# Kernel tuning notes

Measured on AMD Instinct MI355X. Metric: run time of the kernel, lower is better.

The kernel has to match this reference:

```python
import jax, jax.numpy as jnp
import numpy as np

B, N, D, H = 1, 4096, 512, 8
HD = D // H


def setup_inputs() -> dict:
    key = jax.random.key(0)
    ks = jax.random.split(key, 12)
    s = 0.02  # weight init scale for numerical stability
    query = jax.random.normal(ks[0], (B, N, D), jnp.float32)
    key_t = jax.random.normal(ks[1], (B, N, D), jnp.float32)
    value = jax.random.normal(ks[2], (B, N, D), jnp.float32)
    Wq = jax.random.normal(ks[3], (D, D), jnp.float32) * s
    bq = jax.random.normal(ks[4], (D,), jnp.float32) * s
    Wk = jax.random.normal(ks[5], (D, D), jnp.float32) * s
    bk = jax.random.normal(ks[6], (D,), jnp.float32) * s
    Wv = jax.random.normal(ks[7], (D, D), jnp.float32) * s
    bv = jax.random.normal(ks[8], (D,), jnp.float32) * s
    Wo = jax.random.normal(ks[9], (D, D), jnp.float32) * s
    bo = jax.random.normal(ks[10], (D,), jnp.float32) * s
    # build sgconv_mat exactly as __init__: shifted nonneg adjacency, max-normalized,
    # then symmetric degree normalization D^-1/2 A D^-1/2 (gwmha_layer_num=1)
    A = jax.random.uniform(ks[11], (N, N), jnp.float32)
    A = A + A.min()
    A = A / A.max()
    deg = A.sum(1)
    dinv = 1.0 / jnp.sqrt(deg)
    sgconv_mat = (dinv[:, None] * A * dinv[None, :])[None]  # [1,N,N]
    return {"query": query, "key": key_t, "value": value,
            "Wq": Wq, "bq": bq, "Wk": Wk, "bk": bk, "Wv": Wv, "bv": bv,
            "Wo": Wo, "bo": bo, "sgconv_mat": sgconv_mat}


def reference(query, key, value, Wq, bq, Wk, bk, Wv, bv, Wo, bo, sgconv_mat):
    b, n, d = query.shape
    q = (query @ Wq.T + bq).reshape(b, n, H, HD)
    k = (key @ Wk.T + bk).reshape(b, n, H, HD)
    v = (value @ Wv.T + bv).reshape(b, n, H, HD)
    energy = jnp.einsum('bqhd,bkhd->bhqk', q, k)
    attn = jax.nn.softmax(energy / jnp.sqrt(jnp.float32(d)), axis=3)
    out = jnp.einsum('bhqk,bkhd->bqhd', attn, v).reshape(b, n, d)
    out = sgconv_mat @ out          # [1,N,N] @ [B,N,D] -> [B,N,D]
    return out @ Wo.T + bo
```

## Files before the change

### kernel.cpp

```cpp
#include <hip/hip_runtime.h>
#include <hip/hip_bf16.h>
#include <math.h>

typedef __bf16 bf16_t;
typedef __bf16 bf16x8 __attribute__((ext_vector_type(8)));
typedef unsigned short ushort8v __attribute__((ext_vector_type(8)));
typedef float floatx4 __attribute__((ext_vector_type(4)));

static __device__ inline unsigned short f2bf_rne(float f) {
    unsigned int u = __builtin_bit_cast(unsigned int, f);
    unsigned int r = u + 0x7FFFu + ((u >> 16) & 1u);
    return (unsigned short)(r >> 16);
}
static __device__ inline bf16_t f2bf(float f) {
    return __builtin_bit_cast(bf16_t, f2bf_rne(f));
}

static __device__ inline void store_c(float* C, size_t i, float v) { C[i] = v; }
static __device__ inline void store_c(bf16_t* C, size_t i, float v) { C[i] = f2bf(v); }

static __device__ inline void cvt8(const float* src, bf16_t* dst, size_t idx) {
    float4 a = *(const float4*)(src + idx);
    float4 c = *(const float4*)(src + idx + 4);
    ushort8v u;
    u[0] = f2bf_rne(a.x); u[1] = f2bf_rne(a.y); u[2] = f2bf_rne(a.z); u[3] = f2bf_rne(a.w);
    u[4] = f2bf_rne(c.x); u[5] = f2bf_rne(c.y); u[6] = f2bf_rne(c.z); u[7] = f2bf_rne(c.w);
    *(ushort8v*)(dst + idx) = u;
}

template <typename TC>
__device__ inline void gemm_body(
    const bf16_t* __restrict__ A, int lda,
    const bf16_t* __restrict__ B, int ldb,
    const float* __restrict__ bias_col, const float* __restrict__ bias_row,
    TC* __restrict__ C, int ldc, int K, int m0, int n0)
{
    __shared__ bf16_t As[128 * 68];
    __shared__ bf16_t Bs[64 * 68];

    const int tid = threadIdx.x;
    const int lane = tid & 63, wave = tid >> 6;
    const int wm = wave & 1, wn = wave >> 1;
    const int lo16 = lane & 15, quad = lane >> 4;
    const int sr = tid >> 2, sc = (tid & 3) * 8;

    floatx4 acc[4][2] = {};

    for (int k0 = 0; k0 < K; k0 += 32) {
        bf16x8 a0 = *(const bf16x8*)(A + (size_t)(m0 + sr) * lda + k0 + sc);
        bf16x8 a1 = *(const bf16x8*)(A + (size_t)(m0 + 64 + sr) * lda + k0 + sc);
        bf16x8 b0 = *(const bf16x8*)(B + (size_t)(n0 + sr) * ldb + k0 + sc);
        __syncthreads();
        *(bf16x8*)(&As[sr * 68 + sc]) = a0;
        *(bf16x8*)(&As[(64 + sr) * 68 + sc]) = a1;
        *(bf16x8*)(&Bs[sr * 68 + sc]) = b0;
        __syncthreads();

        bf16x8 af[4], bfv[2];
#pragma unroll
        for (int mt = 0; mt < 4; ++mt)
            af[mt] = *(const bf16x8*)(&As[(wm * 64 + mt * 16 + lo16) * 68 + quad * 8]);
#pragma unroll
        for (int nt = 0; nt < 2; ++nt)
            bfv[nt] = *(const bf16x8*)(&Bs[(wn * 32 + nt * 16 + lo16) * 68 + quad * 8]);
#pragma unroll
        for (int mt = 0; mt < 4; ++mt)
#pragma unroll
            for (int nt = 0; nt < 2; ++nt)
                acc[mt][nt] = __builtin_amdgcn_mfma_f32_16x16x32_bf16(
                    af[mt], bfv[nt], acc[mt][nt], 0, 0, 0);
    }

#pragma unroll
    for (int nt = 0; nt < 2; ++nt) {
        const int gn = n0 + wn * 32 + nt * 16 + lo16;
        const float bc = bias_col ? bias_col[gn] : 0.f;
#pragma unroll
        for (int mt = 0; mt < 4; ++mt) {
#pragma unroll
            for (int r = 0; r < 4; ++r) {
                const int gm = m0 + wm * 64 + mt * 16 + quad * 4 + r;
                float v = acc[mt][nt][r] + bc;
                if (bias_row) v += bias_row[gm];
                store_c(C, (size_t)gm * ldc + gn, v);
            }
        }
    }
}

__global__ __launch_bounds__(256) void prep(
    const float* __restrict__ query, const float* __restrict__ key, const float* __restrict__ value,
    const float* __restrict__ Wq, const float* __restrict__ Wk,
    const float* __restrict__ Wv, const float* __restrict__ Wo,
    bf16_t* qB, bf16_t* kB, bf16_t* vB,
    bf16_t* wqB, bf16_t* wkB, bf16_t* wvB, bf16_t* woB)
{
    const int b = blockIdx.x;
    const float* src; bf16_t* dst; size_t base;
    if      (b < 256) { src = query; dst = qB;  base = (size_t)b * 8192; }
    else if (b < 512) { src = key;   dst = kB;  base = (size_t)(b - 256) * 8192; }
    else if (b < 768) { src = value; dst = vB;  base = (size_t)(b - 512) * 8192; }
    else if (b < 800) { src = Wq;    dst = wqB; base = (size_t)(b - 768) * 8192; }
    else if (b < 832) { src = Wk;    dst = wkB; base = (size_t)(b - 800) * 8192; }
    else if (b < 864) { src = Wv;    dst = wvB; base = (size_t)(b - 832) * 8192; }
    else              { src = Wo;    dst = woB; base = (size_t)(b - 864) * 8192; }
#pragma unroll
    for (int it = 0; it < 4; ++it)
        cvt8(src, dst, base + (size_t)it * 2048 + threadIdx.x * 8);
}

__global__ __launch_bounds__(256) void proj_qkv(
    const bf16_t* __restrict__ qB, const bf16_t* __restrict__ wqB, const float* __restrict__ bq,
    const bf16_t* __restrict__ kB, const bf16_t* __restrict__ wkB, const float* __restrict__ bk,
    const bf16_t* __restrict__ wvB, const bf16_t* __restrict__ vB, const float* __restrict__ bv,
    bf16_t* __restrict__ q, bf16_t* __restrict__ k, bf16_t* __restrict__ vt)
{
    const int b = blockIdx.x;
    const bf16_t *A, *B;
    const float *bc = nullptr, *br = nullptr;
    bf16_t* C;
    int ldc = 512, m0, n0;
    if (b < 512) {
        int i = b & 255, x = i & 7, t = i >> 3;
        n0 = (t & 7) * 64;
        m0 = ((t >> 3) * 8 + x) * 128;
        if (b < 256) { A = qB; B = wqB; bc = bq; C = q; }
        else         { A = kB; B = wkB; bc = bk; C = k; }
    } else {
        int i = b - 512;
        n0 = (i & 63) * 64;
        m0 = (i >> 6) * 128;
        A = wvB; B = vB; br = bv; C = vt; ldc = 4096;
    }
    gemm_body<bf16_t>(A, 512, B, 512, bc, br, C, ldc, 512, m0, n0);
}

__global__ __launch_bounds__(256) void sgconv_gemm(
    const bf16_t* __restrict__ sgb, const bf16_t* __restrict__ aot,
    float* __restrict__ part)
{
    const int i = blockIdx.x & 255;
    const int kb = blockIdx.x >> 8;
    const int ms = i & 31, ns = i >> 5;
    const int m0 = ms * 128, n0 = ns * 64;
    const int kbase = kb * 1024;
    gemm_body<float>(sgb + kbase, 4096, aot + kbase, 4096, nullptr, nullptr,
                     part + (size_t)kb * (4096 * 512), 512, 1024, m0, n0);
}

__global__ __launch_bounds__(256) void part_reduce(
    const float* __restrict__ p, bf16_t* __restrict__ o2)
{
    const size_t S = (size_t)4096 * 512;
    const size_t idx = ((size_t)blockIdx.x * 256 + threadIdx.x) * 8;
    ushort8v u;
#pragma unroll
    for (int half = 0; half < 2; ++half) {
        float4 s = *(const float4*)(p + idx + half * 4);
#pragma unroll
        for (int kb = 1; kb < 4; ++kb) {
            float4 t = *(const float4*)(p + kb * S + idx + half * 4);
            s.x += t.x; s.y += t.y; s.z += t.z; s.w += t.w;
        }
        u[half * 4 + 0] = f2bf_rne(s.x);
        u[half * 4 + 1] = f2bf_rne(s.y);
        u[half * 4 + 2] = f2bf_rne(s.z);
        u[half * 4 + 3] = f2bf_rne(s.w);
    }
    *(ushort8v*)(o2 + idx) = u;
}

__global__ __launch_bounds__(256) void out_proj(
    const bf16_t* __restrict__ o2, const bf16_t* __restrict__ woB,
    const float* __restrict__ bo, float* __restrict__ out)
{
    const int i = blockIdx.x, x = i & 7, t = i >> 3;
    const int n0 = (t & 7) * 64;
    const int m0 = ((t >> 3) * 8 + x) * 64;

    __shared__ bf16_t As[64 * 68];
    __shared__ bf16_t Bs[64 * 68];

    const int tid = threadIdx.x;
    const int lane = tid & 63, wave = tid >> 6;
    const int wm = wave & 1, wn = wave >> 1;
    const int lo16 = lane & 15, quad = lane >> 4;
    const int sr = tid >> 2, sc = (tid & 3) * 8;

    floatx4 acc[2][2] = {};

    for (int k0 = 0; k0 < 512; k0 += 32) {
        bf16x8 a0 = *(const bf16x8*)(o2 + (size_t)(m0 + sr) * 512 + k0 + sc);
        bf16x8 b0 = *(const bf16x8*)(woB + (size_t)(n0 + sr) * 512 + k0 + sc);
        __syncthreads();
        *(bf16x8*)(&As[sr * 68 + sc]) = a0;
        *(bf16x8*)(&Bs[sr * 68 + sc]) = b0;
        __syncthreads();

        bf16x8 af[2], bfv[2];
#pragma unroll
        for (int mt = 0; mt < 2; ++mt)
            af[mt] = *(const bf16x8*)(&As[(wm * 32 + mt * 16 + lo16) * 68 + quad * 8]);
#pragma unroll
        for (int nt = 0; nt < 2; ++nt)
            bfv[nt] = *(const bf16x8*)(&Bs[(wn * 32 + nt * 16 + lo16) * 68 + quad * 8]);
#pragma unroll
        for (int mt = 0; mt < 2; ++mt)
#pragma unroll
            for (int nt = 0; nt < 2; ++nt)
                acc[mt][nt] = __builtin_amdgcn_mfma_f32_16x16x32_bf16(
                    af[mt], bfv[nt], acc[mt][nt], 0, 0, 0);
    }

#pragma unroll
    for (int nt = 0; nt < 2; ++nt) {
        const int gn = n0 + wn * 32 + nt * 16 + lo16;
        const float bc = bo[gn];
#pragma unroll
        for (int mt = 0; mt < 2; ++mt)
#pragma unroll
            for (int r = 0; r < 4; ++r) {
                const int gm = m0 + wm * 32 + mt * 16 + quad * 4 + r;
                out[(size_t)gm * 512 + gn] = acc[mt][nt][r] + bc;
            }
    }
}

__global__ __launch_bounds__(256, 4) void flash_attn(
    const bf16_t* __restrict__ q, const bf16_t* __restrict__ kk,
    const bf16_t* __restrict__ vt, float* __restrict__ op,
    float* __restrict__ lp, float scale,
    const float* __restrict__ sg, bf16_t* __restrict__ sgb)
{
    if (blockIdx.x >= 1024) {
        const size_t base = (size_t)(blockIdx.x - 1024) * 8192;
#pragma unroll
        for (int it = 0; it < 4; ++it)
            cvt8(sg, sgb, base + (size_t)it * 2048 + threadIdx.x * 8);
        return;
    }

    const int N = 4096, D = 512;
    const int h   = blockIdx.x & 7;
    const int qb  = (blockIdx.x >> 3) & 31;
    const int qtr = blockIdx.x >> 8;
    const int t0  = qtr * 1024;

    const int tid = threadIdx.x;
    const int w = tid >> 6, lane = tid & 63;
    const int lo16 = lane & 15, quad = lane >> 4;

    __shared__ bf16_t Ks[64 * 72];
    __shared__ bf16_t Vs[64 * 72];
    __shared__ bf16_t Ps[4][32 * 72];

    const bf16_t* qp = q + (size_t)(qb * 128 + w * 32 + lo16) * D + h * 64 + quad * 8;
    bf16x8 qf[2][2];
    qf[0][0] = *(const bf16x8*)qp;
    qf[0][1] = *(const bf16x8*)(qp + 32);
    qf[1][0] = *(const bf16x8*)(qp + 16 * D);
    qf[1][1] = *(const bf16x8*)(qp + 16 * D + 32);

    const int srow = tid >> 2, sc = (tid & 3) * 16;
    const bf16_t* ksrc = kk + (size_t)(t0 + srow) * D + h * 64 + sc;
    const bf16_t* vsrc = vt + (size_t)(h * 64 + srow) * N + t0 + sc;
    bf16_t* kdst = &Ks[srow * 72 + sc];
    bf16_t* vdst = &Vs[srow * 72 + sc];

    floatx4 o[4][2] = {};
    float l[2] = {0.f, 0.f};

    bf16x8 kr0 = *(const bf16x8*)ksrc;
    bf16x8 kr1 = *(const bf16x8*)(ksrc + 8);
    bf16x8 vr0 = *(const bf16x8*)vsrc;
    bf16x8 vr1 = *(const bf16x8*)(vsrc + 8);

    for (int it = 0; it < 16; ++it) {
        __syncthreads();
        *(bf16x8*)kdst = kr0;  *(bf16x8*)(kdst + 8) = kr1;
        *(bf16x8*)vdst = vr0;  *(bf16x8*)(vdst + 8) = vr1;
        __syncthreads();
        if (it < 15) {
            const bf16_t* kn = ksrc + (size_t)(it + 1) * 64 * D;
            const bf16_t* vn = vsrc + (it + 1) * 64;
            kr0 = *(const bf16x8*)kn;  kr1 = *(const bf16x8*)(kn + 8);
            vr0 = *(const bf16x8*)vn;  vr1 = *(const bf16x8*)(vn + 8);
        }

        floatx4 s[4][2];
#pragma unroll
        for (int tt = 0; tt < 4; ++tt) {
            bf16x8 kf0 = *(const bf16x8*)(&Ks[(tt * 16 + lo16) * 72 + quad * 8]);
            bf16x8 kf1 = *(const bf16x8*)(&Ks[(tt * 16 + lo16) * 72 + 32 + quad * 8]);
#pragma unroll
            for (int qt = 0; qt < 2; ++qt) {
                floatx4 a = {};
                a = __builtin_amdgcn_mfma_f32_16x16x32_bf16(kf0, qf[qt][0], a, 0, 0, 0);
                a = __builtin_amdgcn_mfma_f32_16x16x32_bf16(kf1, qf[qt][1], a, 0, 0, 0);
                s[tt][qt] = a;
            }
        }
#pragma unroll
        for (int tt = 0; tt < 4; ++tt)
#pragma unroll
            for (int qt = 0; qt < 2; ++qt) {
                float e0 = __expf(s[tt][qt][0] * scale);
                float e1 = __expf(s[tt][qt][1] * scale);
                float e2 = __expf(s[tt][qt][2] * scale);
                float e3 = __expf(s[tt][qt][3] * scale);
                l[qt] += (e0 + e1) + (e2 + e3);
                uint2 pk;
                pk.x = (unsigned)f2bf_rne(e0) | ((unsigned)f2bf_rne(e1) << 16);
                pk.y = (unsigned)f2bf_rne(e2) | ((unsigned)f2bf_rne(e3) << 16);
                *(uint2*)(&Ps[w][(qt * 16 + lo16) * 72 + tt * 16 + quad * 4]) = pk;
            }
#pragma unroll
        for (int ks = 0; ks < 2; ++ks) {
            bf16x8 pf0 = *(const bf16x8*)(&Ps[w][lo16 * 72 + ks * 32 + quad * 8]);
            bf16x8 pf1 = *(const bf16x8*)(&Ps[w][(16 + lo16) * 72 + ks * 32 + quad * 8]);
#pragma unroll
            for (int t = 0; t < 4; ++t) {
                bf16x8 vf = *(const bf16x8*)(&Vs[(t * 16 + lo16) * 72 + ks * 32 + quad * 8]);
                o[t][0] = __builtin_amdgcn_mfma_f32_16x16x32_bf16(vf, pf0, o[t][0], 0, 0, 0);
                o[t][1] = __builtin_amdgcn_mfma_f32_16x16x32_bf16(vf, pf1, o[t][1], 0, 0, 0);
            }
        }
    }

#pragma unroll
    for (int qt = 0; qt < 2; ++qt) {
        l[qt] += __shfl_xor(l[qt], 16);
        l[qt] += __shfl_xor(l[qt], 32);
    }

    const int g = blockIdx.x & 255;
    float* opw = op + ((size_t)qtr * 256 + g) * 8192;
#pragma unroll
    for (int t = 0; t < 4; ++t)
#pragma unroll
        for (int pt = 0; pt < 2; ++pt)
#pragma unroll
            for (int r = 0; r < 4; ++r)
                opw[(t * 16 + quad * 4 + r) * 128 + w * 32 + pt * 16 + lo16] = o[t][pt][r];

    if (quad == 0) {
        float* lpw = lp + ((size_t)qtr * 256 + g) * 128;
        lpw[w * 32 + lo16] = l[0];
        lpw[w * 32 + 16 + lo16] = l[1];
    }
}

__global__ __launch_bounds__(256) void attn_combine(
    const float* __restrict__ op, const float* __restrict__ lp, bf16_t* __restrict__ aot)
{
    const int g = blockIdx.x;
    const int h = g & 7, qb = g >> 3;
    const int tid = threadIdx.x;
    __shared__ float ls[128];
    if (tid < 128) {
        float s = 0.f;
#pragma unroll
        for (int qtr = 0; qtr < 4; ++qtr)
            s += lp[((size_t)qtr * 256 + g) * 128 + tid];
        ls[tid] = 1.0f / s;
    }
    __syncthreads();
    const float* b0 = op + (size_t)g * 8192;
    const size_t QS = (size_t)256 * 8192;
#pragma unroll 4
    for (int i = 0; i < 32; ++i) {
        int idx = i * 256 + tid;
        float v = b0[idx] + b0[QS + idx] + b0[2 * QS + idx] + b0[3 * QS + idx];
        int dim = idx >> 7, qc = idx & 127;
        aot[(size_t)(h * 64 + dim) * 4096 + qb * 128 + qc] = f2bf(v * ls[qc]);
    }
}

extern "C" void kernel_launch(void* const* d_in, const int* in_sizes, int n_in,
                              void* d_out, int out_size, void* d_ws, size_t ws_size,
                              hipStream_t stream)
{
    const int N = 4096, D = 512;
    const float* query = (const float*)d_in[0];
    const float* key_t = (const float*)d_in[1];
    const float* value = (const float*)d_in[2];
    const float* Wq = (const float*)d_in[3];
    const float* bq = (const float*)d_in[4];
    const float* Wk = (const float*)d_in[5];
    const float* bk = (const float*)d_in[6];
    const float* Wv = (const float*)d_in[7];
    const float* bv = (const float*)d_in[8];
    const float* Wo = (const float*)d_in[9];
    const float* bo = (const float*)d_in[10];
    const float* sg = (const float*)d_in[11];
    float* out = (float*)d_out;

    const size_t ND = (size_t)N * D;
    const size_t DD = (size_t)D * D;

    char* base = (char*)d_ws;
    bf16_t* q    = (bf16_t*)base;
    bf16_t* kk   = q   + ND;
    bf16_t* vt   = kk  + ND;
    bf16_t* aot  = vt  + ND;
    bf16_t* sgb  = aot + ND;
    char* regA   = (char*)(sgb + (size_t)N * N);
    bf16_t* qB   = (bf16_t*)regA;
    bf16_t* kB   = qB + ND;
    bf16_t* vB   = kB + ND;
    bf16_t* wqB  = vB + ND;
    bf16_t* wkB  = wqB + DD;
    bf16_t* wvB  = wkB + DD;
    float* op    = (float*)regA;
    float* p     = (float*)regA;
    char* tail   = regA + (size_t)4 * 256 * 8192 * 4;
    float*  lp   = (float*)tail;
    bf16_t* woB  = (bf16_t*)(lp + (size_t)4 * 256 * 128);
    bf16_t* o2   = woB + DD;

    const dim3 blk(256);

    prep<<<896, blk, 0, stream>>>(query, key_t, value, Wq, Wk, Wv, Wo,
                                  qB, kB, vB, wqB, wkB, wvB, woB);

    proj_qkv<<<768, blk, 0, stream>>>(qB, wqB, bq, kB, wkB, bk,
                                      wvB, vB, bv, q, kk, vt);

    const float scale = 1.0f / sqrtf((float)D);
    flash_attn<<<3072, blk, 0, stream>>>(q, kk, vt, op, lp, scale, sg, sgb);
    attn_combine<<<256, blk, 0, stream>>>(op, lp, aot);

    sgconv_gemm<<<1024, blk, 0, stream>>>(sgb, aot, p);
    part_reduce<<<1024, blk, 0, stream>>>(p, o2);
    out_proj<<<512, blk, 0, stream>>>(o2, woB, bo, out);

    (void)in_sizes; (void)n_in; (void)out_size; (void)ws_size;
}
```

Measured before the change: 252.8 us.

## Use 128x128 GEMM tiles with direct global-to-LDS loads and fold softmax scale

The shared GEMM body now computes 128x128 tiles. It loads operands straight into LDS with global_load_lds, using an XOR-swizzled layout in place of the padded one, and halves the grid sizes for the projection and sgconv GEMMs. The softmax scale and log2(e) are folded into the Q projection, so the attention kernel uses exp2f without a per-element multiply. The hand-written RNE bf16 conversion is swapped for native casts, and the sgconv conversion blocks are interleaved with flash-attention blocks. Larger tiles raise register use and halve the number of workgroups, which could reduce occupancy.

Result: slower. 278.5 us (+10.2%).

```diff
diff --git a/kernel.cpp b/kernel.cpp
--- a/kernel.cpp
+++ b/kernel.cpp
@@ -4,76 +4,101 @@
 
 typedef __bf16 bf16_t;
 typedef __bf16 bf16x8 __attribute__((ext_vector_type(8)));
-typedef unsigned short ushort8v __attribute__((ext_vector_type(8)));
 typedef float floatx4 __attribute__((ext_vector_type(4)));
 
-static __device__ inline unsigned short f2bf_rne(float f) {
-    unsigned int u = __builtin_bit_cast(unsigned int, f);
-    unsigned int r = u + 0x7FFFu + ((u >> 16) & 1u);
-    return (unsigned short)(r >> 16);
-}
-static __device__ inline bf16_t f2bf(float f) {
-    return __builtin_bit_cast(bf16_t, f2bf_rne(f));
+typedef __attribute__((address_space(1))) void gvoid_t;
+typedef __attribute__((address_space(3))) void lvoid_t;
+
+static __device__ __forceinline__ void gload_lds16(const bf16_t* g, const bf16_t* l) {
+    __builtin_amdgcn_global_load_lds((gvoid_t*)(size_t)g,
+                                     (lvoid_t*)(unsigned)(size_t)l,
+                                     16, 0, 0);
+}
+
+static __device__ __forceinline__ unsigned pack_bf2(float lo, float hi) {
+    bf16_t a = (bf16_t)lo, b = (bf16_t)hi;
+    return (unsigned)__builtin_bit_cast(unsigned short, a)
+         | ((unsigned)__builtin_bit_cast(unsigned short, b) << 16);
 }
 
 static __device__ inline void store_c(float* C, size_t i, float v) { C[i] = v; }
-static __device__ inline void store_c(bf16_t* C, size_t i, float v) { C[i] = f2bf(v); }
+static __device__ inline void store_c(bf16_t* C, size_t i, float v) { C[i] = (bf16_t)v; }
 
 static __device__ inline void cvt8(const float* src, bf16_t* dst, size_t idx) {
     float4 a = *(const float4*)(src + idx);
     float4 c = *(const float4*)(src + idx + 4);
-    ushort8v u;
-    u[0] = f2bf_rne(a.x); u[1] = f2bf_rne(a.y); u[2] = f2bf_rne(a.z); u[3] = f2bf_rne(a.w);
-    u[4] = f2bf_rne(c.x); u[5] = f2bf_rne(c.y); u[6] = f2bf_rne(c.z); u[7] = f2bf_rne(c.w);
-    *(ushort8v*)(dst + idx) = u;
+    uint4 u;
+    u.x = pack_bf2(a.x, a.y);
+    u.y = pack_bf2(a.z, a.w);
+    u.z = pack_bf2(c.x, c.y);
+    u.w = pack_bf2(c.z, c.w);
+    *(uint4*)(dst + idx) = u;
 }
 
 template <typename TC>
-__device__ inline void gemm_body(
+__device__ inline void gemm_body128(
     const bf16_t* __restrict__ A, int lda,
     const bf16_t* __restrict__ B, int ldb,
     const float* __restrict__ bias_col, const float* __restrict__ bias_row,
+    float cscale,
     TC* __restrict__ C, int ldc, int K, int m0, int n0)
 {
-    __shared__ bf16_t As[128 * 68];
-    __shared__ bf16_t Bs[64 * 68];
+    __shared__ bf16_t As[128 * 32];
+    __shared__ bf16_t Bs[128 * 32];
 
     const int tid = threadIdx.x;
     const int lane = tid & 63, wave = tid >> 6;
     const int wm = wave & 1, wn = wave >> 1;
     const int lo16 = lane & 15, quad = lane >> 4;
-    const int sr = tid >> 2, sc = (tid & 3) * 8;
-
-    floatx4 acc[4][2] = {};
+
+    const int r0 = tid >> 2;
+    const int s0 = tid & 3;
+    const int c0 = s0 ^ ((r0 >> 1) & 3);
+    const bf16_t* ga0 = A + (size_t)(m0 + r0) * lda + c0 * 8;
+    const bf16_t* ga1 = A + (size_t)(m0 + 64 + r0) * lda + c0 * 8;
+    const bf16_t* gb0 = B + (size_t)(n0 + r0) * ldb + c0 * 8;
+    const bf16_t* gb1 = B + (size_t)(n0 + 64 + r0) * ldb + c0 * 8;
+    const bf16_t* la0 = As + wave * 512;
+    const bf16_t* la1 = As + 2048 + wave * 512;
+    const bf16_t* lb0 = Bs + wave * 512;
+    const bf16_t* lb1 = Bs + 2048 + wave * 512;
+
+    int aoff[4], boff[4];
+#pragma unroll
+    for (int t = 0; t < 4; ++t) {
+        const int ra = wm * 64 + t * 16 + lo16;
+        aoff[t] = ra * 32 + ((quad ^ ((ra >> 1) & 3)) << 3);
+        const int rb = wn * 64 + t * 16 + lo16;
+        boff[t] = rb * 32 + ((quad ^ ((rb >> 1) & 3)) << 3);
+    }
+
+    floatx4 acc[4][4] = {};
 
     for (int k0 = 0; k0 < K; k0 += 32) {
-        bf16x8 a0 = *(const bf16x8*)(A + (size_t)(m0 + sr) * lda + k0 + sc);
-        bf16x8 a1 = *(const bf16x8*)(A + (size_t)(m0 + 64 + sr) * lda + k0 + sc);
-        bf16x8 b0 = *(const bf16x8*)(B + (size_t)(n0 + sr) * ldb + k0 + sc);
-        __syncthreads();
-        *(bf16x8*)(&As[sr * 68 + sc]) = a0;
-        *(bf16x8*)(&As[(64 + sr) * 68 + sc]) = a1;
-        *(bf16x8*)(&Bs[sr * 68 + sc]) = b0;
-        __syncthreads();
-
-        bf16x8 af[4], bfv[2];
+        __syncthreads();
+        gload_lds16(ga0 + k0, la0);
+        gload_lds16(ga1 + k0, la1);
+        gload_lds16(gb0 + k0, lb0);
+        gload_lds16(gb1 + k0, lb1);
+        __syncthreads();
+
+        bf16x8 af[4], bfv[4];
+#pragma unroll
+        for (int t = 0; t < 4; ++t) {
+            af[t]  = *(const bf16x8*)(As + aoff[t]);
+            bfv[t] = *(const bf16x8*)(Bs + boff[t]);
+        }
 #pragma unroll
         for (int mt = 0; mt < 4; ++mt)
-            af[mt] = *(const bf16x8*)(&As[(wm * 64 + mt * 16 + lo16) * 68 + quad * 8]);
-#pragma unroll
-        for (int nt = 0; nt < 2; ++nt)
-            bfv[nt] = *(const bf16x8*)(&Bs[(wn * 32 + nt * 16 + lo16) * 68 + quad * 8]);
-#pragma unroll
-        for (int mt = 0; mt < 4; ++mt)
-#pragma unroll
-            for (int nt = 0; nt < 2; ++nt)
+#pragma unroll
+            for (int nt = 0; nt < 4; ++nt)
                 acc[mt][nt] = __builtin_amdgcn_mfma_f32_16x16x32_bf16(
                     af[mt], bfv[nt], acc[mt][nt], 0, 0, 0);
     }
 
 #pragma unroll
-    for (int nt = 0; nt < 2; ++nt) {
-        const int gn = n0 + wn * 32 + nt * 16 + lo16;
+    for (int nt = 0; nt < 4; ++nt) {
+        const int gn = n0 + wn * 64 + nt * 16 + lo16;
         const float bc = bias_col ? bias_col[gn] : 0.f;
 #pragma unroll
         for (int mt = 0; mt < 4; ++mt) {
@@ -82,7 +107,7 @@
                 const int gm = m0 + wm * 64 + mt * 16 + quad * 4 + r;
                 float v = acc[mt][nt][r] + bc;
                 if (bias_row) v += bias_row[gm];
-                store_c(C, (size_t)gm * ldc + gn, v);
+                store_c(C, (size_t)gm * ldc + gn, v * cscale);
             }
         }
     }
@@ -113,39 +138,32 @@
     const bf16_t* __restrict__ qB, const bf16_t* __restrict__ wqB, const float* __restrict__ bq,
     const bf16_t* __restrict__ kB, const bf16_t* __restrict__ wkB, const float* __restrict__ bk,
     const bf16_t* __restrict__ wvB, const bf16_t* __restrict__ vB, const float* __restrict__ bv,
-    bf16_t* __restrict__ q, bf16_t* __restrict__ k, bf16_t* __restrict__ vt)
+    bf16_t* __restrict__ q, bf16_t* __restrict__ k, bf16_t* __restrict__ vt, float qscale)
 {
     const int b = blockIdx.x;
-    const bf16_t *A, *B;
-    const float *bc = nullptr, *br = nullptr;
-    bf16_t* C;
-    int ldc = 512, m0, n0;
-    if (b < 512) {
-        int i = b & 255, x = i & 7, t = i >> 3;
-        n0 = (t & 7) * 64;
-        m0 = ((t >> 3) * 8 + x) * 128;
-        if (b < 256) { A = qB; B = wqB; bc = bq; C = q; }
-        else         { A = kB; B = wkB; bc = bk; C = k; }
+    const int i = b & 127;
+    if (b < 256) {
+        const int m0 = (i & 31) * 128, n0 = (i >> 5) * 128;
+        if (b < 128)
+            gemm_body128<bf16_t>(qB, 512, wqB, 512, bq, nullptr, qscale, q, 512, 512, m0, n0);
+        else
+            gemm_body128<bf16_t>(kB, 512, wkB, 512, bk, nullptr, 1.f, k, 512, 512, m0, n0);
     } else {
-        int i = b - 512;
-        n0 = (i & 63) * 64;
-        m0 = (i >> 6) * 128;
-        A = wvB; B = vB; br = bv; C = vt; ldc = 4096;
-    }
-    gemm_body<bf16_t>(A, 512, B, 512, bc, br, C, ldc, 512, m0, n0);
+        const int m0 = (i & 3) * 128, n0 = (i >> 2) * 128;
+        gemm_body128<bf16_t>(wvB, 512, vB, 512, nullptr, bv, 1.f, vt, 4096, 512, m0, n0);
+    }
 }
 
 __global__ __launch_bounds__(256) void sgconv_gemm(
     const bf16_t* __restrict__ sgb, const bf16_t* __restrict__ aot,
     float* __restrict__ part)
 {
-    const int i = blockIdx.x & 255;
-    const int kb = blockIdx.x >> 8;
-    const int ms = i & 31, ns = i >> 5;
-    const int m0 = ms * 128, n0 = ns * 64;
+    const int i = blockIdx.x & 127;
+    const int kb = blockIdx.x >> 7;
+    const int m0 = (i & 31) * 128, n0 = (i >> 5) * 128;
     const int kbase = kb * 1024;
-    gemm_body<float>(sgb + kbase, 4096, aot + kbase, 4096, nullptr, nullptr,
-                     part + (size_t)kb * (4096 * 512), 512, 1024, m0, n0);
+    gemm_body128<float>(sgb + kbase, 4096, aot + kbase, 4096, nullptr, nullptr, 1.f,
+                        part + (size_t)kb * (4096 * 512), 512, 1024, m0, n0);
 }
 
 __global__ __launch_bounds__(256) void part_reduce(
@@ -153,7 +171,7 @@
 {
     const size_t S = (size_t)4096 * 512;
     const size_t idx = ((size_t)blockIdx.x * 256 + threadIdx.x) * 8;
-    ushort8v u;
+    uint4 u;
 #pragma unroll
     for (int half = 0; half < 2; ++half) {
         float4 s = *(const float4*)(p + idx + half * 4);
@@ -162,12 +180,10 @@
             float4 t = *(const float4*)(p + kb * S + idx + half * 4);
             s.x += t.x; s.y += t.y; s.z += t.z; s.w += t.w;
         }
-        u[half * 4 + 0] = f2bf_rne(s.x);
-        u[half * 4 + 1] = f2bf_rne(s.y);
-        u[half * 4 + 2] = f2bf_rne(s.z);
-        u[half * 4 + 3] = f2bf_rne(s.w);
-    }
-    *(ushort8v*)(o2 + idx) = u;
+        if (half == 0) { u.x = pack_bf2(s.x, s.y); u.y = pack_bf2(s.z, s.w); }
+        else           { u.z = pack_bf2(s.x, s.y); u.w = pack_bf2(s.z, s.w); }
+    }
+    *(uint4*)(o2 + idx) = u;
 }
 
 __global__ __launch_bounds__(256) void out_proj(
@@ -229,21 +245,24 @@
 __global__ __launch_bounds__(256, 4) void flash_attn(
     const bf16_t* __restrict__ q, const bf16_t* __restrict__ kk,
     const bf16_t* __restrict__ vt, float* __restrict__ op,
-    float* __restrict__ lp, float scale,
+    float* __restrict__ lp,
     const float* __restrict__ sg, bf16_t* __restrict__ sgb)
 {
-    if (blockIdx.x >= 1024) {
-        const size_t base = (size_t)(blockIdx.x - 1024) * 8192;
+    const unsigned bid = blockIdx.x;
+    const unsigned rm = bid % 3u;
+    if (rm) {
+        const size_t base = (size_t)((bid / 3u) * 2u + (rm - 1u)) * 8192;
 #pragma unroll
         for (int it = 0; it < 4; ++it)
             cvt8(sg, sgb, base + (size_t)it * 2048 + threadIdx.x * 8);
         return;
     }
+    const int fid = bid / 3u;
 
     const int N = 4096, D = 512;
-    const int h   = blockIdx.x & 7;
-    const int qb  = (blockIdx.x >> 3) & 31;
-    const int qtr = blockIdx.x >> 8;
+    const int h   = fid & 7;
+    const int qb  = (fid >> 3) & 31;
+    const int qtr = fid >> 8;
     const int t0  = qtr * 1024;
 
     const int tid = threadIdx.x;
@@ -304,14 +323,14 @@
         for (int tt = 0; tt < 4; ++tt)
 #pragma unroll
             for (int qt = 0; qt < 2; ++qt) {
-                float e0 = __expf(s[tt][qt][0] * scale);
-                float e1 = __expf(s[tt][qt][1] * scale);
-                float e2 = __expf(s[tt][qt][2] * scale);
-                float e3 = __expf(s[tt][qt][3] * scale);
+                float e0 = exp2f(s[tt][qt][0]);
+                float e1 = exp2f(s[tt][qt][1]);
+                float e2 = exp2f(s[tt][qt][2]);
+                float e3 = exp2f(s[tt][qt][3]);
                 l[qt] += (e0 + e1) + (e2 + e3);
                 uint2 pk;
-                pk.x = (unsigned)f2bf_rne(e0) | ((unsigned)f2bf_rne(e1) << 16);
-                pk.y = (unsigned)f2bf_rne(e2) | ((unsigned)f2bf_rne(e3) << 16);
+                pk.x = pack_bf2(e0, e1);
+                pk.y = pack_bf2(e2, e3);
                 *(uint2*)(&Ps[w][(qt * 16 + lo16) * 72 + tt * 16 + quad * 4]) = pk;
             }
 #pragma unroll
@@ -333,7 +352,7 @@
         l[qt] += __shfl_xor(l[qt], 32);
     }
 
-    const int g = blockIdx.x & 255;
+    const int g = fid & 255;
     float* opw = op + ((size_t)qtr * 256 + g) * 8192;
 #pragma unroll
     for (int t = 0; t < 4; ++t)
@@ -372,7 +391,7 @@
         int idx = i * 256 + tid;
         float v = b0[idx] + b0[QS + idx] + b0[2 * QS + idx] + b0[3 * QS + idx];
         int dim = idx >> 7, qc = idx & 127;
-        aot[(size_t)(h * 64 + dim) * 4096 + qb * 128 + qc] = f2bf(v * ls[qc]);
+        aot[(size_t)(h * 64 + dim) * 4096 + qb * 128 + qc] = (bf16_t)(v * ls[qc]);
     }
 }
 
@@ -423,14 +442,14 @@
     prep<<<896, blk, 0, stream>>>(query, key_t, value, Wq, Wk, Wv, Wo,
                                   qB, kB, vB, wqB, wkB, wvB, woB);
 
-    proj_qkv<<<768, blk, 0, stream>>>(qB, wqB, bq, kB, wkB, bk,
-                                      wvB, vB, bv, q, kk, vt);
-
-    const float scale = 1.0f / sqrtf((float)D);
-    flash_attn<<<3072, blk, 0, stream>>>(q, kk, vt, op, lp, scale, sg, sgb);
+    const float qscale = 1.44269504088896f / sqrtf((float)D);
+    proj_qkv<<<384, blk, 0, stream>>>(qB, wqB, bq, kB, wkB, bk,
+                                      wvB, vB, bv, q, kk, vt, qscale);
+
+    flash_attn<<<3072, blk, 0, stream>>>(q, kk, vt, op, lp, sg, sgb);
     attn_combine<<<256, blk, 0, stream>>>(op, lp, aot);
 
-    sgconv_gemm<<<1024, blk, 0, stream>>>(sgb, aot, p);
+    sgconv_gemm<<<512, blk, 0, stream>>>(sgb, aot, p);
     part_reduce<<<1024, blk, 0, stream>>>(p, o2);
     out_proj<<<512, blk, 0, stream>>>(o2, woB, bo, out);
 
```
